# Performance work log

Measured on AMD Instinct MI355X. Metric: run time of the kernel, lower is better.

The kernel has to match this reference:

```python
import jax, jax.numpy as jnp
import numpy as np


def _rgcn(x, src, dst, et, basis, comp, root, bias):
    # Basis-decomposed RGCNConv (PyG semantics): per-relation mean aggregation
    # over incoming edges + root transform + bias.
    N = x.shape[0]
    R = comp.shape[0]
    W = jnp.einsum('rb,bio->rio', comp, basis)          # [R, in, out]
    xr = jnp.einsum('ni,rio->rno', x, W)                 # [R, N, out]
    msg = xr[et, src]                                    # [E, out] gather per edge
    seg = dst * R + et                                   # (target, relation) segment id
    cnt = jax.ops.segment_sum(jnp.ones(et.shape, x.dtype), seg, num_segments=N * R)
    norm = 1.0 / jnp.maximum(cnt, 1.0)                   # mean per (dst, relation)
    msg = msg * norm[seg][:, None]
    agg = jax.ops.segment_sum(msg, dst, num_segments=N)  # scatter-add to targets
    return agg + x @ root + bias


def setup_inputs() -> dict:
    key = jax.random.key(0)
    ks = jax.random.split(key, 20)
    N, E, R, B, F, D, C, NB = 100000, 1600000, 5, 512, 4, 32, 5, 2
    s = 0.1
    inp = {
        'x': jax.random.normal(ks[0], (N, F), jnp.float32),
        'edge_index': jax.random.randint(ks[1], (2, E), 0, N, dtype=jnp.int32),
        'edge_type': jax.random.randint(ks[2], (E,), 0, R, dtype=jnp.int32),
        'start_nodes': jax.random.randint(ks[3], (B,), 0, N, dtype=jnp.int32),
        # layer 0: in=F, out=D
        'basis0': jax.random.normal(ks[4], (NB, F, D), jnp.float32) * s,
        'comp0': jax.random.normal(ks[5], (R, NB), jnp.float32) * s,
        'root0': jax.random.normal(ks[6], (F, D), jnp.float32) * s,
        'bias0': jax.random.normal(ks[7], (D,), jnp.float32) * s,
        # layers 1..3: in=out=D, stacked
        'basis': jax.random.normal(ks[8], (3, NB, D, D), jnp.float32) * s,
        'comp': jax.random.normal(ks[9], (3, R, NB), jnp.float32) * s,
        'root': jax.random.normal(ks[10], (3, D, D), jnp.float32) * s,
        'bias': jax.random.normal(ks[11], (3, D), jnp.float32) * s,
        # MLP head: sum(latent_dim)=128 -> 128 -> C
        'lin1_w': jax.random.normal(ks[12], (4 * D, 128), jnp.float32) * s,
        'lin1_b': jax.random.normal(ks[13], (128,), jnp.float32) * s,
        'lin2_w': jax.random.normal(ks[14], (128, C), jnp.float32) * s,
        'lin2_b': jax.random.normal(ks[15], (C,), jnp.float32) * s,
    }
    return inp


def reference(x, edge_index, edge_type, start_nodes, basis0, comp0, root0, bias0,
              basis, comp, root, bias, lin1_w, lin1_b, lin2_w, lin2_b):
    src, dst = edge_index[0], edge_index[1]
    h = jnp.tanh(_rgcn(x, src, dst, edge_type, basis0, comp0, root0, bias0))
    states = [h]
    for l in range(basis.shape[0]):
        h = jnp.tanh(_rgcn(h, src, dst, edge_type, basis[l], comp[l], root[l], bias[l]))
        states.append(h)
    concat = jnp.concatenate(states, axis=1)             # [N, 128]
    # Per-graph readout: the walk's degenerate n_walks=1 branch, i.e. the
    # start (user) node's concatenated state (sequential backtracking walk
    # replaced by its deterministic initialization path; eval mode, no dropout).
    acc = concat[start_nodes]                            # [B, 128]
    h1 = jax.nn.relu(acc @ lin1_w + lin1_b)
    logits = h1 @ lin2_w + lin2_b
    return jax.nn.log_softmax(logits, axis=-1)
```

## Files before the change

kernel.cpp:

```cpp
#include <hip/hip_runtime.h>
#include <cstdint>

#define N_NODES 100000
#define N_EDGES 1600000
#define R_REL   5
#define NBASIS  2
#define B_START 512
#define PART_SZ 12500
#define NBUCK   256
#define BUCK_SZ 391
#define EPB     6250
#define STAGE_CAP 7000
#define UNR     32
#define NBLK32  3125

typedef __attribute__((ext_vector_type(8))) short short8;
typedef __attribute__((ext_vector_type(4))) float f32x4;
typedef _Float16 half8 __attribute__((ext_vector_type(8)));
typedef unsigned uint32x2 __attribute__((ext_vector_type(2)));
typedef unsigned uint32x4 __attribute__((ext_vector_type(4)));

__device__ __forceinline__ unsigned short f2bf(float f) {
    unsigned u = __float_as_uint(f);
    unsigned r = (u + 0x7FFF + ((u >> 16) & 1)) >> 16;
    return (unsigned short)r;
}
__device__ __forceinline__ float bf2f(unsigned short u) {
    return __uint_as_float(((unsigned)u) << 16);
}
__device__ __forceinline__ unsigned short f2h(float f) {
    _Float16 h = (_Float16)f;
    return __builtin_bit_cast(unsigned short, h);
}


__global__ __launch_bounds__(256) void k_cntb(
    const int* __restrict__ ei, int* __restrict__ bhist) {
    __shared__ int lh[NBUCK];
    int tid = threadIdx.x;
    lh[tid] = 0;
    __syncthreads();
    int base = blockIdx.x * EPB;
    for (int j = tid; j < EPB; j += 256) {
        int dst = ei[N_EDGES + base + j];
        atomicAdd(&lh[dst / BUCK_SZ], 1);
    }
    __syncthreads();
    bhist[blockIdx.x * NBUCK + tid] = lh[tid];
}

__global__ __launch_bounds__(256) void k_colscan(
    int* __restrict__ bhist, int* __restrict__ colsum) {
    __shared__ int s[256];
    int b = blockIdx.x, i = threadIdx.x;
    int v = bhist[i * NBUCK + b];
    s[i] = v;
    __syncthreads();
    for (int o = 1; o < 256; o <<= 1) {
        int t = (i >= o) ? s[i - o] : 0;
        __syncthreads();
        s[i] += t;
        __syncthreads();
    }
    bhist[i * NBUCK + b] = s[i] - v;
    if (i == 255) colsum[b] = s[255];
}

__global__ __launch_bounds__(256) void k_tiny(
    const int* __restrict__ colsum, int* __restrict__ bbase) {
    __shared__ int s[256];
    int i = threadIdx.x;
    int v = colsum[i];
    s[i] = v;
    __syncthreads();
    for (int o = 1; o < 256; o <<= 1) {
        int t = (i >= o) ? s[i - o] : 0;
        __syncthreads();
        s[i] += t;
        __syncthreads();
    }
    bbase[i] = s[i] - v;
    if (i == 255) bbase[NBUCK] = s[255];
}

__global__ __launch_bounds__(256) void k_scat(
    const int* __restrict__ ei, const int* __restrict__ et,
    const int* __restrict__ bhist, const int* __restrict__ bbase,
    int* __restrict__ arena) {
    __shared__ int lc[NBUCK];
    int tid = threadIdx.x;
    lc[tid] = bhist[blockIdx.x * NBUCK + tid] + bbase[tid];
    __syncthreads();
    int base = blockIdx.x * EPB;
    for (int j = tid; j < EPB; j += 256) {
        int e   = base + j;
        int src = ei[e];
        int dst = ei[N_EDGES + e];
        int t   = et[e];
        int bk  = dst / BUCK_SZ;
        int dl  = dst - bk * BUCK_SZ;
        int pos = atomicAdd(&lc[bk], 1);
        arena[pos] = src | (t << 17) | (dl << 20);
    }
}

__global__ __launch_bounds__(256) void k_build(
    const int* __restrict__ arena, const int* __restrict__ bbase,
    int* __restrict__ off, int* __restrict__ pk_m, float* __restrict__ nv5,
    unsigned* __restrict__ degpk) {
    __shared__ int deg5[BUCK_SZ * R_REL];
    __shared__ int loff[BUCK_SZ + 1];
    __shared__ int cur5[BUCK_SZ * R_REL];
    __shared__ int stg[STAGE_CAP];
    __shared__ int tsum[256];
    int b = blockIdx.x, tid = threadIdx.x;
    int base = bbase[b], end = bbase[b + 1];
    int count = end - base;
    for (int i = tid; i < BUCK_SZ * R_REL; i += 256) deg5[i] = 0;
    __syncthreads();
    for (int i = tid; i < count; i += 256) {
        int r  = arena[base + i];
        int dl = ((unsigned)r) >> 20;
        int t  = (r >> 17) & 7;
        atomicAdd(&deg5[dl * R_REL + t], 1);
    }
    __syncthreads();
    for (int dl = tid; dl < BUCK_SZ; dl += 256) {
        loff[dl] = deg5[dl * R_REL + 0] + deg5[dl * R_REL + 1] +
                   deg5[dl * R_REL + 2] + deg5[dl * R_REL + 3] +
                   deg5[dl * R_REL + 4];
    }
    __syncthreads();
    int d0 = 2 * tid, d1 = 2 * tid + 1;
    int va = (d0 < BUCK_SZ) ? loff[d0] : 0;
    int vb = (d1 < BUCK_SZ) ? loff[d1] : 0;
    tsum[tid] = va + vb;
    __syncthreads();
    for (int o = 1; o < 256; o <<= 1) {
        int v = (tid >= o) ? tsum[tid - o] : 0;
        __syncthreads();
        tsum[tid] += v;
        __syncthreads();
    }
    int pre = tsum[tid] - (va + vb);
    if (d0 < BUCK_SZ) loff[d0] = pre;
    if (d1 < BUCK_SZ) loff[d1] = pre + va;
    __syncthreads();
    for (int dl = tid; dl < BUCK_SZ; dl += 256) {
        int nn = b * BUCK_SZ + dl;
        int run = loff[dl];
        unsigned dp = 0;
#pragma unroll
        for (int t = 0; t < R_REL; t++) {
            cur5[dl * R_REL + t] = run;
            int c = deg5[dl * R_REL + t];
            run += c;
            int cc = c > 63 ? 63 : c;
            dp |= ((unsigned)cc) << (6 * t);
        }
        if (nn < N_NODES) {
            off[nn]   = base + loff[dl];
            degpk[nn] = dp;
#pragma unroll
            for (int t = 0; t < R_REL; t++) {
                int c = deg5[dl * R_REL + t];
                nv5[nn * R_REL + t] = 1.0f / (float)(c > 0 ? c : 1);
            }
        }
    }
    if (b == NBUCK - 1 && tid == 0) off[N_NODES] = N_EDGES;
    __syncthreads();
    for (int i = tid; i < count; i += 256) {
        int r  = arena[base + i];
        int dl = ((unsigned)r) >> 20;
        int t  = (r >> 17) & 7;
        int rk = atomicAdd(&cur5[dl * R_REL + t], 1);
        if (rk < STAGE_CAP) stg[rk] = r;
    }
    __syncthreads();
    for (int i = tid; i < count; i += 256) {
        int r = stg[i < STAGE_CAP ? i : STAGE_CAP - 1];
        pk_m[base + i] = r & 0x1FFFF;
    }
}


__global__ __launch_bounds__(256) void k_wprep(
    const float* __restrict__ basis, const float* __restrict__ comp,
    const float* __restrict__ root,  const float* __restrict__ basis0,
    const float* __restrict__ comp0, const float* __restrict__ root0,
    unsigned short* __restrict__ wfh, unsigned short* __restrict__ wfr,
    unsigned short* __restrict__ wf0) {
    __shared__ float lw[5120];
    int tid = threadIdx.x;
    int l = blockIdx.x;
    if (l < 3) {
        for (int idx = tid; idx < 5120; idx += 256) {
            int r = idx >> 10, rem = idx & 1023, i = rem >> 5, o = rem & 31;
            lw[idx] = comp[l * 10 + r * 2 + 0] * basis[l * 2048 + i * 32 + o]
                    + comp[l * 10 + r * 2 + 1] * basis[l * 2048 + 1024 + i * 32 + o];
        }
        __syncthreads();
        for (int idx = tid; idx < 5120; idx += 256) {
            int ot = idx / 2560, rem = idx % 2560;
            int s = rem >> 9, ln = (rem >> 3) & 63, j = idx & 7;
            int o = ot * 16 + (ln & 15), kk = (ln >> 4) * 8 + j;
            wfh[l * 5120 + idx] = f2h(lw[s * 1024 + kk * 32 + o]);
        }
        for (int idx = tid; idx < 2048; idx += 256) {
            int ot = idx >> 10, s = (idx >> 9) & 1, ln = (idx >> 3) & 63, j = idx & 7;
            int o = ot * 16 + (ln & 15), kk = (ln >> 4) * 8 + j;
            float val = root[l * 1024 + kk * 32 + o];
            unsigned short hi = f2bf(val);
            wfr[l * 2048 + idx] = s ? f2bf(val - bf2f(hi)) : hi;
        }
    } else {
        for (int idx = tid; idx < 1024; idx += 256) {
            int k = idx >> 5, o = idx & 31;
            float val = 0.f;
            if (k < 20) {
                int r = k >> 2, i = k & 3;
                val = comp0[r * 2 + 0] * basis0[i * 32 + o]
                    + comp0[r * 2 + 1] * basis0[128 + i * 32 + o];
            } else if (k < 24) val = root0[(k - 20) * 32 + o];
            lw[idx] = val;
        }
        __syncthreads();
        for (int idx = tid; idx < 1024; idx += 256) {
            int ot = idx >> 9, ln = (idx >> 3) & 63, j = idx & 7;
            int o = ot * 16 + (ln & 15), kk = (ln >> 4) * 8 + j;
            wf0[idx] = f2h(lw[kk * 32 + o]);
        }
    }
}


__global__ __launch_bounds__(128) void k_gath32(
    const unsigned short* __restrict__ hb, const int* __restrict__ pk_m,
    const float* __restrict__ nv5, const unsigned* __restrict__ degpk,
    const int* __restrict__ off, unsigned short* __restrict__ agg,
    const float* __restrict__ h, const int* __restrict__ start,
    float* __restrict__ sav, int slot) {
    int tid = threadIdx.x;
    if (blockIdx.x >= NBLK32) {
        int idx = (blockIdx.x - NBLK32) * 128 + tid;
        int b = idx >> 5, ln = idx & 31;
        sav[(size_t)slot * 16384 + idx] = h[(size_t)start[b] * 32 + ln];
        return;
    }
    int n = blockIdx.x * 32 + (tid >> 2);
    int cpos = tid & 3;
    const uint32x4* __restrict__ hb4 = (const uint32x4*)hb;

    int e0 = off[n];
    unsigned dp = degpk[n];
    int b1 = dp & 63;
    int b2 = b1 + ((dp >> 6) & 63);
    int b3 = b2 + ((dp >> 12) & 63);
    int b4 = b3 + ((dp >> 18) & 63);
    int deg = b4 + ((dp >> 24) & 63);
    float nv0 = nv5[n * R_REL + 0];
    float nv1 = nv5[n * R_REL + 1];
    float nv2 = nv5[n * R_REL + 2];
    float nv3 = nv5[n * R_REL + 3];
    float nv4 = nv5[n * R_REL + 4];

    int m[UNR];
#pragma unroll
    for (int k = 0; k < UNR; k++) {
        m[k] = 0;
        if (k < deg) m[k] = __builtin_nontemporal_load(pk_m + e0 + k);
    }

    float a[R_REL][8];
#pragma unroll
    for (int r = 0; r < R_REL; r++)
#pragma unroll
        for (int j = 0; j < 8; j++) a[r][j] = 0.f;

#pragma unroll
    for (int k = 0; k < UNR; k++) {
        if (k < deg) {
            uint32x4 u = hb4[(size_t)m[k] * 4 + cpos];
            float v[8];
            v[0] = __uint_as_float(u.x << 16);
            v[1] = __uint_as_float(u.x & 0xFFFF0000u);
            v[2] = __uint_as_float(u.y << 16);
            v[3] = __uint_as_float(u.y & 0xFFFF0000u);
            v[4] = __uint_as_float(u.z << 16);
            v[5] = __uint_as_float(u.z & 0xFFFF0000u);
            v[6] = __uint_as_float(u.w << 16);
            v[7] = __uint_as_float(u.w & 0xFFFF0000u);
            float w[R_REL];
            w[0] = (k < b1) ? nv0 : 0.f;
            w[1] = (k >= b1 && k < b2) ? nv1 : 0.f;
            w[2] = (k >= b2 && k < b3) ? nv2 : 0.f;
            w[3] = (k >= b3 && k < b4) ? nv3 : 0.f;
            w[4] = (k >= b4) ? nv4 : 0.f;
#pragma unroll
            for (int r = 0; r < R_REL; r++)
#pragma unroll
                for (int j = 0; j < 8; j++) a[r][j] += w[r] * v[j];
        }
    }
    for (int k = UNR; k < deg; k++) {
        int mk = __builtin_nontemporal_load(pk_m + e0 + k);
        uint32x4 u = hb4[(size_t)mk * 4 + cpos];
        float v[8];
        v[0] = __uint_as_float(u.x << 16);
        v[1] = __uint_as_float(u.x & 0xFFFF0000u);
        v[2] = __uint_as_float(u.y << 16);
        v[3] = __uint_as_float(u.y & 0xFFFF0000u);
        v[4] = __uint_as_float(u.z << 16);
        v[5] = __uint_as_float(u.z & 0xFFFF0000u);
        v[6] = __uint_as_float(u.w << 16);
        v[7] = __uint_as_float(u.w & 0xFFFF0000u);
        float w[R_REL];
        w[0] = (k < b1) ? nv0 : 0.f;
        w[1] = (k >= b1 && k < b2) ? nv1 : 0.f;
        w[2] = (k >= b2 && k < b3) ? nv2 : 0.f;
        w[3] = (k >= b3 && k < b4) ? nv3 : 0.f;
        w[4] = (k >= b4) ? nv4 : 0.f;
#pragma unroll
        for (int r = 0; r < R_REL; r++)
#pragma unroll
            for (int j = 0; j < 8; j++) a[r][j] += w[r] * v[j];
    }
#pragma unroll
    for (int r = 0; r < R_REL; r++) {
        uint32x4 pk;
        pk.x = (unsigned)f2h(a[r][0]) | ((unsigned)f2h(a[r][1]) << 16);
        pk.y = (unsigned)f2h(a[r][2]) | ((unsigned)f2h(a[r][3]) << 16);
        pk.z = (unsigned)f2h(a[r][4]) | ((unsigned)f2h(a[r][5]) << 16);
        pk.w = (unsigned)f2h(a[r][6]) | ((unsigned)f2h(a[r][7]) << 16);
        __builtin_nontemporal_store(pk,
            (uint32x4*)(agg + (size_t)n * 160 + r * 32 + cpos * 8));
    }
}


__global__ __launch_bounds__(256) void k_gath0(
    const float* __restrict__ x, const int* __restrict__ pk_m,
    const float* __restrict__ nv5, const unsigned* __restrict__ degpk,
    const int* __restrict__ off, unsigned short* __restrict__ a0v) {
    int tid  = threadIdx.x;
    int lane32 = tid & 31;
    int sub  = tid >> 5;
    int part  = blockIdx.x & 7;
    int local = (blockIdx.x >> 3) * 8 + sub;
    if (local >= PART_SZ) return;
    int n = part * PART_SZ + local;
    int cpos = lane32 & 1;
    int slot = lane32 >> 1;
    const float2* __restrict__ x2 = (const float2*)x;

    int e0 = off[n];
    unsigned dp = degpk[n];
    int chunkbase = e0;
    int mreg = (chunkbase + lane32 < N_EDGES)
             ? __builtin_nontemporal_load(pk_m + chunkbase + lane32) : 0;
    int e = e0;
#pragma unroll
    for (int r = 0; r < R_REL; r++) {
        int cnt = (int)((dp >> (6 * r)) & 63u);
        float nv = nv5[n * R_REL + r];
        float p0 = 0.f, p1 = 0.f;
        for (int kb = 0; kb < cnt; kb += 16) {
            if (e + kb + 15 >= chunkbase + 32) {
                chunkbase = e + kb;
                mreg = (chunkbase + lane32 < N_EDGES)
                     ? __builtin_nontemporal_load(pk_m + chunkbase + lane32) : 0;
            }
            int kq = kb + slot;
            int mq = __shfl(mreg, e + kq - chunkbase, 32);
            float2 u = x2[(size_t)mq * 2 + cpos];
            float msk = (kq < cnt) ? nv : 0.f;
            p0 += msk * u.x;
            p1 += msk * u.y;
        }
        e += cnt;
        p0 += __shfl_xor(p0, 2, 32); p0 += __shfl_xor(p0, 4, 32);
        p0 += __shfl_xor(p0, 8, 32); p0 += __shfl_xor(p0, 16, 32);
        p1 += __shfl_xor(p1, 2, 32); p1 += __shfl_xor(p1, 4, 32);
        p1 += __shfl_xor(p1, 8, 32); p1 += __shfl_xor(p1, 16, 32);
        if (slot == 0) {
            unsigned pk = (unsigned)f2h(p0) | ((unsigned)f2h(p1) << 16);
            *(unsigned*)(a0v + (size_t)n * 32 + r * 4 + cpos * 2) = pk;
        }
    }
    if (lane32 < 12) {
        float xv = (lane32 < 4) ? x[(size_t)n * 4 + lane32] : 0.f;
        a0v[(size_t)n * 32 + 20 + lane32] = (lane32 < 4) ? f2h(xv) : (unsigned short)0;
    }
}


__global__ __launch_bounds__(256) void k_gemm(
    const unsigned short* __restrict__ agg, const unsigned short* __restrict__ hbin,
    const unsigned short* __restrict__ wfhl, const unsigned short* __restrict__ wfrl,
    const float* __restrict__ biasL, float* __restrict__ h,
    unsigned short* __restrict__ hbout) {
    int tid = threadIdx.x;
    int wid = tid >> 6, lane = tid & 63;
    int tile = blockIdx.x * 4 + wid;
    if (tile >= N_NODES / 16) return;
    int n0 = tile * 16;
    int row = lane & 15, kg = lane >> 4;
    const half8* ar = (const half8*)(agg + (size_t)(n0 + row) * 160 + kg * 8);
    const half8* wh = (const half8*)wfhl;
    const short8* wr = (const short8*)wfrl;
    short8 hbf = *(const short8*)(hbin + (size_t)(n0 + row) * 32 + kg * 8);
    f32x4 c0 = {0.f, 0.f, 0.f, 0.f}, c1 = {0.f, 0.f, 0.f, 0.f};
#pragma unroll
    for (int s = 0; s < 5; s++) {
        half8 a = __builtin_nontemporal_load(&ar[s * 4]);
        c0 = __builtin_amdgcn_mfma_f32_16x16x32_f16(a, wh[s * 64 + lane], c0, 0, 0, 0);
        c1 = __builtin_amdgcn_mfma_f32_16x16x32_f16(a, wh[320 + s * 64 + lane], c1, 0, 0, 0);
    }
    c0 = __builtin_amdgcn_mfma_f32_16x16x32_bf16(hbf, wr[lane], c0, 0, 0, 0);
    c0 = __builtin_amdgcn_mfma_f32_16x16x32_bf16(hbf, wr[64 + lane], c0, 0, 0, 0);
    c1 = __builtin_amdgcn_mfma_f32_16x16x32_bf16(hbf, wr[128 + lane], c1, 0, 0, 0);
    c1 = __builtin_amdgcn_mfma_f32_16x16x32_bf16(hbf, wr[192 + lane], c1, 0, 0, 0);
    float b0 = biasL[row], b1 = biasL[16 + row];
#pragma unroll
    for (int i = 0; i < 4; i++) {
        int n = n0 + kg * 4 + i;
        float t0 = tanhf(c0[i] + b0);
        float t1 = tanhf(c1[i] + b1);
        h[(size_t)n * 32 + row]      = t0;
        h[(size_t)n * 32 + 16 + row] = t1;
        hbout[(size_t)n * 32 + row]      = f2bf(t0);
        hbout[(size_t)n * 32 + 16 + row] = f2bf(t1);
    }
}

__global__ __launch_bounds__(256) void k_gemm0(
    const unsigned short* __restrict__ a0v, const unsigned short* __restrict__ wf0,
    const float* __restrict__ biasL, float* __restrict__ h,
    unsigned short* __restrict__ hbout) {
    int tid = threadIdx.x;
    int wid = tid >> 6, lane = tid & 63;
    int tile = blockIdx.x * 4 + wid;
    if (tile >= N_NODES / 16) return;
    int n0 = tile * 16;
    int row = lane & 15, kg = lane >> 4;
    half8 a = *(const half8*)(a0v + (size_t)(n0 + row) * 32 + kg * 8);
    const half8* wv = (const half8*)wf0;
    f32x4 c0 = {0.f, 0.f, 0.f, 0.f}, c1 = {0.f, 0.f, 0.f, 0.f};
    c0 = __builtin_amdgcn_mfma_f32_16x16x32_f16(a, wv[lane], c0, 0, 0, 0);
    c1 = __builtin_amdgcn_mfma_f32_16x16x32_f16(a, wv[64 + lane], c1, 0, 0, 0);
    float b0 = biasL[row], b1 = biasL[16 + row];
#pragma unroll
    for (int i = 0; i < 4; i++) {
        int n = n0 + kg * 4 + i;
        float t0 = tanhf(c0[i] + b0);
        float t1 = tanhf(c1[i] + b1);
        h[(size_t)n * 32 + row]      = t0;
        h[(size_t)n * 32 + 16 + row] = t1;
        hbout[(size_t)n * 32 + row]      = f2bf(t0);
        hbout[(size_t)n * 32 + 16 + row] = f2bf(t1);
    }
}


__global__ __launch_bounds__(128) void k_mlp(
    const float* __restrict__ sav, const float* __restrict__ h,
    const int* __restrict__ start, const float* __restrict__ w1,
    const float* __restrict__ b1, const float* __restrict__ w2,
    const float* __restrict__ b2, float* __restrict__ out) {
    __shared__ float cvec[128];
    __shared__ float hb[128];
    __shared__ float lg[8];
    int b = blockIdx.x, t = threadIdx.x;
    int l = t >> 5, ln = t & 31;
    cvec[t] = (l < 3) ? sav[l * (B_START * 32) + b * 32 + ln]
                      : h[(size_t)start[b] * 32 + ln];
    __syncthreads();
    float a = b1[t];
#pragma unroll 8
    for (int k = 0; k < 128; k++) a += cvec[k] * w1[k * 128 + t];
    hb[t] = fmaxf(a, 0.f);
    __syncthreads();
    if (t < 5) {
        float a2 = b2[t];
        for (int k = 0; k < 128; k++) a2 += hb[k] * w2[k * 5 + t];
        lg[t] = a2;
    }
    __syncthreads();
    if (t < 5) {
        float m = lg[0];
        for (int j = 1; j < 5; j++) m = fmaxf(m, lg[j]);
        float s = 0.f;
        for (int j = 0; j < 5; j++) s += expf(lg[j] - m);
        out[b * 5 + t] = lg[t] - m - logf(s);
    }
}


extern "C" void kernel_launch(void* const* d_in, const int* in_sizes, int n_in,
                              void* d_out, int out_size, void* d_ws, size_t ws_size,
                              hipStream_t stream) {
    const float* x      = (const float*)d_in[0];
    const int*   ei     = (const int*)d_in[1];
    const int*   etype  = (const int*)d_in[2];
    const int*   start  = (const int*)d_in[3];
    const float* basis0 = (const float*)d_in[4];
    const float* comp0  = (const float*)d_in[5];
    const float* root0  = (const float*)d_in[6];
    const float* bias0  = (const float*)d_in[7];
    const float* basis  = (const float*)d_in[8];
    const float* comp   = (const float*)d_in[9];
    const float* root   = (const float*)d_in[10];
    const float* bias   = (const float*)d_in[11];
    const float* w1     = (const float*)d_in[12];
    const float* b1     = (const float*)d_in[13];
    const float* w2     = (const float*)d_in[14];
    const float* b2     = (const float*)d_in[15];
    float* out = (float*)d_out;

    char* p = (char*)d_ws;
    auto alloc = [&](size_t bytes) -> void* {
        void* r = (void*)p;
        p += (bytes + 255) & ~(size_t)255;
        return r;
    };
    int*            bhist  = (int*)alloc((size_t)NBUCK * NBUCK * 4);
    int*            colsum = (int*)alloc(NBUCK * 4);
    int*            bbase  = (int*)alloc((NBUCK + 1) * 4);
    int*            arena  = (int*)alloc((size_t)N_EDGES * 4);
    int*            off    = (int*)alloc((N_NODES + 1) * 4);
    int*            pk_m   = (int*)alloc((size_t)N_EDGES * 4);
    float*          nv5    = (float*)alloc((size_t)N_NODES * R_REL * 4);
    unsigned*       degpk  = (unsigned*)alloc((size_t)N_NODES * 4);
    float*          h      = (float*)alloc((size_t)N_NODES * 32 * 4);
    unsigned short* hbuf   = (unsigned short*)alloc((size_t)(N_NODES + 64) * 32 * 2);
    unsigned short* a0v    = (unsigned short*)alloc((size_t)(N_NODES + 64) * 32 * 2);
    unsigned short* agg    = (unsigned short*)alloc((size_t)(N_NODES + 64) * 160 * 2);
    unsigned short* wfh    = (unsigned short*)alloc((size_t)3 * 5120 * 2);
    unsigned short* wfr    = (unsigned short*)alloc((size_t)3 * 2048 * 2);
    unsigned short* wf0    = (unsigned short*)alloc((size_t)1024 * 2);
    float*          sav    = (float*)alloc(4 * B_START * 32 * 4);

    k_cntb<<<NBUCK, 256, 0, stream>>>(ei, bhist);
    k_colscan<<<NBUCK, 256, 0, stream>>>(bhist, colsum);
    k_tiny<<<1, 256, 0, stream>>>(colsum, bbase);
    k_scat<<<NBUCK, 256, 0, stream>>>(ei, etype, bhist, bbase, arena);
    k_build<<<NBUCK, 256, 0, stream>>>(arena, bbase, off, pk_m, nv5, degpk);
    k_wprep<<<4, 256, 0, stream>>>(basis, comp, root, basis0, comp0, root0,
                                   wfh, wfr, wf0);

    int nbGath0 = 8 * ((PART_SZ + 7) / 8);
    int nbGemm  = (N_NODES / 16 + 3) / 4;
    int nbG32   = NBLK32 + 128;

    k_gath0<<<nbGath0, 256, 0, stream>>>(x, pk_m, nv5, degpk, off, a0v);
    k_gemm0<<<nbGemm, 256, 0, stream>>>(a0v, wf0, bias0, h, hbuf);
    for (int l = 0; l < 3; l++) {
        k_gath32<<<nbG32, 128, 0, stream>>>(hbuf, pk_m, nv5, degpk, off, agg,
                                            h, start, sav, l);
        k_gemm<<<nbGemm, 256, 0, stream>>>(agg, hbuf, wfh + (size_t)l * 5120,
                                           wfr + (size_t)l * 2048, bias + l * 32,
                                           h, hbuf);
    }

    k_mlp<<<B_START, 128, 0, stream>>>(sav, h, start, w1, b1, w2, b2, out);
}
```

Baseline: 387.2 us.

## Replace bucketed two-pass CSR build with global atomic counting sort

The CSR build previously bucketed edges by destination, scattered them to an arena, then sorted each bucket per (dst, relation) in shared memory. It now counts edges per (dst, relation) with global atomics, scans those counts into offsets, and scatters source ids straight into their final positions with global atomics. This removes the arena pass and the shared-memory staging, but relies on heavy global atomic traffic. Edge order within a (dst, relation) segment is no longer deterministic, which can change floating-point summation order.

```diff
diff --git a/kernel.cpp b/kernel.cpp
--- a/kernel.cpp
+++ b/kernel.cpp
@@ -7,12 +7,10 @@
 #define NBASIS  2
 #define B_START 512
 #define PART_SZ 12500
-#define NBUCK   256
 #define BUCK_SZ 391
-#define EPB     6250
-#define STAGE_CAP 7000
 #define UNR     32
 #define NBLK32  3125
+#define NC5     500224
 
 typedef __attribute__((ext_vector_type(8))) short short8;
 typedef __attribute__((ext_vector_type(4))) float f32x4;
@@ -34,101 +32,63 @@
 }
 
 
-__global__ __launch_bounds__(256) void k_cntb(
-    const int* __restrict__ ei, int* __restrict__ bhist) {
-    __shared__ int lh[NBUCK];
-    int tid = threadIdx.x;
-    lh[tid] = 0;
-    __syncthreads();
-    int base = blockIdx.x * EPB;
-    for (int j = tid; j < EPB; j += 256) {
-        int dst = ei[N_EDGES + base + j];
-        atomicAdd(&lh[dst / BUCK_SZ], 1);
-    }
-    __syncthreads();
-    bhist[blockIdx.x * NBUCK + tid] = lh[tid];
-}
-
-__global__ __launch_bounds__(256) void k_colscan(
-    int* __restrict__ bhist, int* __restrict__ colsum) {
+__global__ __launch_bounds__(256) void k_zero(int* __restrict__ cnt5) {
+    cnt5[blockIdx.x * 256 + threadIdx.x] = 0;
+}
+
+__global__ __launch_bounds__(256) void k_cnt2(
+    const int* __restrict__ ei, const int* __restrict__ et,
+    int* __restrict__ cnt5) {
+    int e = blockIdx.x * 256 + threadIdx.x;
+    int dst = ei[N_EDGES + e];
+    int t   = et[e];
+    atomicAdd(&cnt5[dst * R_REL + t], 1);
+}
+
+__global__ __launch_bounds__(256) void k_scanA(
+    const int* __restrict__ cnt5, int* __restrict__ blocksum) {
     __shared__ int s[256];
-    int b = blockIdx.x, i = threadIdx.x;
-    int v = bhist[i * NBUCK + b];
-    s[i] = v;
-    __syncthreads();
-    for (int o = 1; o < 256; o <<= 1) {
-        int t = (i >= o) ? s[i - o] : 0;
-        __syncthreads();
-        s[i] += t;
-        __syncthreads();
-    }
-    bhist[i * NBUCK + b] = s[i] - v;
-    if (i == 255) colsum[b] = s[255];
-}
-
-__global__ __launch_bounds__(256) void k_tiny(
-    const int* __restrict__ colsum, int* __restrict__ bbase) {
-    __shared__ int s[256];
-    int i = threadIdx.x;
-    int v = colsum[i];
-    s[i] = v;
-    __syncthreads();
-    for (int o = 1; o < 256; o <<= 1) {
-        int t = (i >= o) ? s[i - o] : 0;
-        __syncthreads();
-        s[i] += t;
-        __syncthreads();
-    }
-    bbase[i] = s[i] - v;
-    if (i == 255) bbase[NBUCK] = s[255];
-}
-
-__global__ __launch_bounds__(256) void k_scat(
-    const int* __restrict__ ei, const int* __restrict__ et,
-    const int* __restrict__ bhist, const int* __restrict__ bbase,
-    int* __restrict__ arena) {
-    __shared__ int lc[NBUCK];
-    int tid = threadIdx.x;
-    lc[tid] = bhist[blockIdx.x * NBUCK + tid] + bbase[tid];
-    __syncthreads();
-    int base = blockIdx.x * EPB;
-    for (int j = tid; j < EPB; j += 256) {
-        int e   = base + j;
-        int src = ei[e];
-        int dst = ei[N_EDGES + e];
-        int t   = et[e];
-        int bk  = dst / BUCK_SZ;
-        int dl  = dst - bk * BUCK_SZ;
-        int pos = atomicAdd(&lc[bk], 1);
-        arena[pos] = src | (t << 17) | (dl << 20);
-    }
-}
-
-__global__ __launch_bounds__(256) void k_build(
-    const int* __restrict__ arena, const int* __restrict__ bbase,
-    int* __restrict__ off, int* __restrict__ pk_m, float* __restrict__ nv5,
+    int b = blockIdx.x, tid = threadIdx.x;
+    int lo = b * (BUCK_SZ * R_REL);
+    int hi = lo + BUCK_SZ * R_REL;
+    if (hi > N_NODES * R_REL) hi = N_NODES * R_REL;
+    int acc = 0;
+    for (int i = lo + tid; i < hi; i += 256) acc += cnt5[i];
+    s[tid] = acc;
+    __syncthreads();
+    for (int o = 128; o > 0; o >>= 1) {
+        if (tid < o) s[tid] += s[tid + o];
+        __syncthreads();
+    }
+    if (tid == 0) blocksum[b] = s[0];
+}
+
+__global__ __launch_bounds__(256) void k_scanB(
+    const int* __restrict__ blocksum, int* __restrict__ cnt5,
+    int* __restrict__ off, float* __restrict__ nv5,
     unsigned* __restrict__ degpk) {
-    __shared__ int deg5[BUCK_SZ * R_REL];
+    __shared__ int s2[256];
     __shared__ int loff[BUCK_SZ + 1];
-    __shared__ int cur5[BUCK_SZ * R_REL];
-    __shared__ int stg[STAGE_CAP];
     __shared__ int tsum[256];
     int b = blockIdx.x, tid = threadIdx.x;
-    int base = bbase[b], end = bbase[b + 1];
-    int count = end - base;
-    for (int i = tid; i < BUCK_SZ * R_REL; i += 256) deg5[i] = 0;
-    __syncthreads();
-    for (int i = tid; i < count; i += 256) {
-        int r  = arena[base + i];
-        int dl = ((unsigned)r) >> 20;
-        int t  = (r >> 17) & 7;
-        atomicAdd(&deg5[dl * R_REL + t], 1);
-    }
-    __syncthreads();
+    int bself = blocksum[b];
+    s2[tid] = blocksum[tid];
+    __syncthreads();
+    for (int o = 1; o < 256; o <<= 1) {
+        int v = (tid >= o) ? s2[tid - o] : 0;
+        __syncthreads();
+        s2[tid] += v;
+        __syncthreads();
+    }
+    int base = s2[b] - bself;
     for (int dl = tid; dl < BUCK_SZ; dl += 256) {
-        loff[dl] = deg5[dl * R_REL + 0] + deg5[dl * R_REL + 1] +
-                   deg5[dl * R_REL + 2] + deg5[dl * R_REL + 3] +
-                   deg5[dl * R_REL + 4];
+        int n = b * BUCK_SZ + dl;
+        int d = 0;
+        if (n < N_NODES) {
+#pragma unroll
+            for (int t = 0; t < R_REL; t++) d += cnt5[n * R_REL + t];
+        }
+        loff[dl] = d;
     }
     __syncthreads();
     int d0 = 2 * tid, d1 = 2 * tid + 1;
@@ -147,41 +107,35 @@
     if (d1 < BUCK_SZ) loff[d1] = pre + va;
     __syncthreads();
     for (int dl = tid; dl < BUCK_SZ; dl += 256) {
-        int nn = b * BUCK_SZ + dl;
-        int run = loff[dl];
-        unsigned dp = 0;
-#pragma unroll
-        for (int t = 0; t < R_REL; t++) {
-            cur5[dl * R_REL + t] = run;
-            int c = deg5[dl * R_REL + t];
-            run += c;
-            int cc = c > 63 ? 63 : c;
-            dp |= ((unsigned)cc) << (6 * t);
-        }
-        if (nn < N_NODES) {
-            off[nn]   = base + loff[dl];
-            degpk[nn] = dp;
+        int n = b * BUCK_SZ + dl;
+        if (n < N_NODES) {
+            int run = base + loff[dl];
+            off[n] = run;
+            unsigned dp = 0;
 #pragma unroll
             for (int t = 0; t < R_REL; t++) {
-                int c = deg5[dl * R_REL + t];
-                nv5[nn * R_REL + t] = 1.0f / (float)(c > 0 ? c : 1);
+                int c = cnt5[n * R_REL + t];
+                cnt5[n * R_REL + t] = run;
+                run += c;
+                int cc = c > 63 ? 63 : c;
+                dp |= ((unsigned)cc) << (6 * t);
+                nv5[n * R_REL + t] = 1.0f / (float)(c > 0 ? c : 1);
             }
-        }
-    }
-    if (b == NBUCK - 1 && tid == 0) off[N_NODES] = N_EDGES;
-    __syncthreads();
-    for (int i = tid; i < count; i += 256) {
-        int r  = arena[base + i];
-        int dl = ((unsigned)r) >> 20;
-        int t  = (r >> 17) & 7;
-        int rk = atomicAdd(&cur5[dl * R_REL + t], 1);
-        if (rk < STAGE_CAP) stg[rk] = r;
-    }
-    __syncthreads();
-    for (int i = tid; i < count; i += 256) {
-        int r = stg[i < STAGE_CAP ? i : STAGE_CAP - 1];
-        pk_m[base + i] = r & 0x1FFFF;
-    }
+            degpk[n] = dp;
+        }
+    }
+    if (b == 255 && tid == 0) off[N_NODES] = N_EDGES;
+}
+
+__global__ __launch_bounds__(256) void k_scat2(
+    const int* __restrict__ ei, const int* __restrict__ et,
+    int* __restrict__ cnt5, int* __restrict__ pk_m) {
+    int e = blockIdx.x * 256 + threadIdx.x;
+    int src = ei[e];
+    int dst = ei[N_EDGES + e];
+    int t   = et[e];
+    int pos = atomicAdd(&cnt5[dst * R_REL + t], 1);
+    __builtin_nontemporal_store(src, pk_m + pos);
 }
 
 
@@ -524,10 +478,8 @@
         p += (bytes + 255) & ~(size_t)255;
         return r;
     };
-    int*            bhist  = (int*)alloc((size_t)NBUCK * NBUCK * 4);
-    int*            colsum = (int*)alloc(NBUCK * 4);
-    int*            bbase  = (int*)alloc((NBUCK + 1) * 4);
-    int*            arena  = (int*)alloc((size_t)N_EDGES * 4);
+    int*            cnt5   = (int*)alloc((size_t)NC5 * 4);
+    int*            bsum   = (int*)alloc(256 * 4);
     int*            off    = (int*)alloc((N_NODES + 1) * 4);
     int*            pk_m   = (int*)alloc((size_t)N_EDGES * 4);
     float*          nv5    = (float*)alloc((size_t)N_NODES * R_REL * 4);
@@ -541,11 +493,11 @@
     unsigned short* wf0    = (unsigned short*)alloc((size_t)1024 * 2);
     float*          sav    = (float*)alloc(4 * B_START * 32 * 4);
 
-    k_cntb<<<NBUCK, 256, 0, stream>>>(ei, bhist);
-    k_colscan<<<NBUCK, 256, 0, stream>>>(bhist, colsum);
-    k_tiny<<<1, 256, 0, stream>>>(colsum, bbase);
-    k_scat<<<NBUCK, 256, 0, stream>>>(ei, etype, bhist, bbase, arena);
-    k_build<<<NBUCK, 256, 0, stream>>>(arena, bbase, off, pk_m, nv5, degpk);
+    k_zero <<<NC5 / 256, 256, 0, stream>>>(cnt5);
+    k_cnt2 <<<N_EDGES / 256, 256, 0, stream>>>(ei, etype, cnt5);
+    k_scanA<<<256, 256, 0, stream>>>(cnt5, bsum);
+    k_scanB<<<256, 256, 0, stream>>>(bsum, cnt5, off, nv5, degpk);
+    k_scat2<<<N_EDGES / 256, 256, 0, stream>>>(ei, etype, cnt5, pk_m);
     k_wprep<<<4, 256, 0, stream>>>(basis, comp, root, basis0, comp0, root0,
                                    wfh, wfr, wf0);
 
```

Result: slower. 538.4 us (+39.0%).
